# Kernel tuning notes

Measured on AMD Instinct MI355X. Metric: run time of the kernel, lower is better.

The kernel has to match this reference:

```python
import jax, jax.numpy as jnp
import numpy as np
import math

B = 16384
INPUT = 2048
HIDDEN = 2048
PROJ = 1024


def setup_inputs() -> dict:
    key = jax.random.key(0)
    ks = jax.random.split(key, 20)
    stdv = 1.0 / math.sqrt(PROJ)
    u = lambda k, shape: jax.random.uniform(k, shape, jnp.float32, -stdv, stdv)
    return {
        "x_t": jax.random.normal(ks[0], (B, INPUT), jnp.float32),
        "h_t": jax.random.normal(ks[1], (B, PROJ), jnp.float32),
        "c_t": jax.random.normal(ks[2], (B, HIDDEN), jnp.float32),
        "weight_if_x": u(ks[3], (INPUT, 2 * HIDDEN)),
        "weight_if_h": u(ks[4], (PROJ, 2 * HIDDEN)),
        "weight_if_c": u(ks[5], (HIDDEN, 2 * HIDDEN)),
        "bias_i": u(ks[6], (HIDDEN,)),
        "bias_f": u(ks[7], (HIDDEN,)),
        "weight_c_x": u(ks[8], (INPUT, HIDDEN)),
        "weight_c_h": u(ks[9], (PROJ, HIDDEN)),
        "bias_c": u(ks[10], (HIDDEN,)),
        "weight_o_x": u(ks[11], (INPUT, PROJ)),
        "weight_o_h": u(ks[12], (PROJ, PROJ)),
        "weight_o_c": u(ks[13], (HIDDEN, PROJ)),
        "bias_o": u(ks[14], (PROJ,)),
        "weight_r_proj": u(ks[15], (HIDDEN, PROJ)),
        "weight_r_x": u(ks[16], (INPUT, PROJ)),
    }


def reference(x_t, h_t, c_t, weight_if_x, weight_if_h, weight_if_c, bias_i, bias_f,
              weight_c_x, weight_c_h, bias_c, weight_o_x, weight_o_h, weight_o_c,
              bias_o, weight_r_proj, weight_r_x):
    # input/forget gates with peephole on c_t: [B, 2*HIDDEN]
    if_gates = x_t @ weight_if_x + h_t @ weight_if_h + c_t @ weight_if_c
    ingate, forgetgate = jnp.split(if_gates, 2, axis=-1)
    ingate = jax.nn.sigmoid(ingate + bias_i)
    forgetgate = jax.nn.sigmoid(forgetgate + bias_f)
    cellgate = jnp.tanh(x_t @ weight_c_x + h_t @ weight_c_h + bias_c)
    c_new = forgetgate * c_t + ingate * cellgate
    # output gate peeps at new cell state
    outgate = jax.nn.sigmoid(x_t @ weight_o_x + h_t @ weight_o_h + c_new @ weight_o_c + bias_o)
    r_t = jnp.tanh(c_new)
    m_t = r_t @ weight_r_proj
    # input_size != proj_size -> project x for the residual connection
    h_new = outgate * (m_t + x_t @ weight_r_x)
    return (h_new, c_new)
```

## Files before the change

kernel.cpp:

```cpp
#include <hip/hip_runtime.h>
#include <hip/hip_bf16.h>
#include <math.h>

typedef unsigned short u16;
typedef __bf16 bf16x8_t __attribute__((ext_vector_type(8)));
typedef float  f32x4_t  __attribute__((ext_vector_type(4)));
typedef float  f32x8_t  __attribute__((ext_vector_type(8)));
typedef float  f32x16_t __attribute__((ext_vector_type(16)));
typedef u16    u16x4_t  __attribute__((ext_vector_type(4)));
typedef u16    u16x8_t  __attribute__((ext_vector_type(8)));

__device__ __forceinline__ u16 f2b(float f) {
  unsigned u = __builtin_bit_cast(unsigned, f);
  u += 0x7fffu + ((u >> 16) & 1u);
  return (u16)(u >> 16);
}
__device__ __forceinline__ float b2f(u16 h) {
  unsigned u = ((unsigned)h) << 16;
  return __builtin_bit_cast(float, u);
}
__device__ __forceinline__ float sigm_(float x) { return 1.0f / (1.0f + __expf(-x)); }
__device__ __forceinline__ float tanh_(float x) { return 1.0f - 2.0f / (__expf(2.0f * x) + 1.0f); }

__device__ __forceinline__ void gload16(const void* g, void* l) {
  __builtin_amdgcn_global_load_lds(
      (__attribute__((address_space(1))) void*)(g),
      (__attribute__((address_space(3))) void*)(l), 16, 0, 0);
}


__global__ void cvt_act_kernel(const float* __restrict__ src, u16* __restrict__ dst,
                               int C, int KT, int c0) {
  int mb = blockIdx.x, ktl = blockIdx.y, t = threadIdx.x;
  int ktg = (c0 >> 5) + ktl;
  const float* s = src + (long)(mb * 256 + t) * C + ktl * 32;
  u16* d = dst + ((long)(mb * KT + ktg)) * 8192 + t * 8;
#pragma unroll
  for (int p = 0; p < 4; ++p) {
    f32x8_t v = *(const f32x8_t*)(s + p * 8);
    u16x8_t o;
#pragma unroll
    for (int r = 0; r < 8; ++r) o[r] = f2b(v[r]);
    *(u16x8_t*)(d + p * 2048) = o;
  }
}

__global__ void cvt_wt_kernel(const float* __restrict__ src, u16* __restrict__ dst,
                              int N, int KT, int n0, int k0) {
  int bx = blockIdx.x, by = blockIdx.y, t = threadIdx.x;
  int n = bx * 256 + t;
  int nb_g = (n0 >> 8) + bx;
  int ktg = (k0 >> 5) + by;
  float tmp[32];
#pragma unroll
  for (int kk = 0; kk < 32; ++kk)
    tmp[kk] = src[(long)(by * 32 + kk) * N + n];
  u16* d = dst + ((long)(nb_g * KT + ktg)) * 8192 + t * 8;
#pragma unroll
  for (int p = 0; p < 4; ++p) {
    u16x8_t o;
#pragma unroll
    for (int r = 0; r < 8; ++r) o[r] = f2b(tmp[p * 8 + r]);
    *(u16x8_t*)(d + p * 2048) = o;
  }
}

template <int MODE>
__global__ __launch_bounds__(512, 2) void gemm256_kernel(
    const u16* __restrict__ A, const u16* __restrict__ Bt, u16* __restrict__ Cout) {
  constexpr int KTF  = (MODE == 0) ? 160 : 128;
  constexpr int NCOL = (MODE == 0) ? 8192 : 2048;
  constexpr int NBN  = NCOL / 256;

  __shared__ u16 lds[2 * 32768];

  int bid = blockIdx.x;
  int cpx = gridDim.x >> 3;
  bid = (bid & 7) * cpx + (bid >> 3);

  int mb = bid / NBN, nb = bid % NBN;
  int m0 = mb * 256, n0 = nb * 256;

  int kt0, NT;
  if (MODE == 0) { kt0 = 0; NT = (nb < 16) ? 80 : ((nb < 28) ? 48 : 32); }
  else           { kt0 = (nb < 4) ? 0 : 64; NT = 32; }

  const int tid  = threadIdx.x;
  const int lane = tid & 63;
  const int wid  = tid >> 6;
  const int wr   = wid >> 2;
  const int wc   = wid & 3;
  const int l31  = lane & 31;
  const int hl   = lane >> 5;

  const int dstg = tid * 8;
  const u16* pA = A  + ((long)(mb * KTF + kt0)) * 8192 + dstg;
  const u16* pB = Bt + ((long)(nb * KTF + kt0)) * 8192 + dstg;

#define STG(bufb, tt, g) do { \
    gload16(pA + ((long)(2 * (tt))) * 8192 + (g) * 4096, \
            &lds[(bufb) * 32768 + (g) * 4096 + dstg]); \
    gload16(pB + ((long)(2 * (tt))) * 8192 + (g) * 4096, \
            &lds[(bufb) * 32768 + 16384 + (g) * 4096 + dstg]); } while (0)

  const int xbase = (wr * 128 + l31) * 8;
  const int wbase = (wc * 64  + l31) * 8;

  struct Frag { bf16x8_t x0, x1, x2, x3, w0, w1; };
  Frag fA, fB;

#define RD(F, sbp, ks) do { \
    const u16* _t = (sbp) + (2 * (ks) + hl) * 2048; \
    F.x0 = *(const bf16x8_t*)(_t + xbase); \
    F.x1 = *(const bf16x8_t*)(_t + xbase + 256); \
    F.x2 = *(const bf16x8_t*)(_t + xbase + 512); \
    F.x3 = *(const bf16x8_t*)(_t + xbase + 768); \
    F.w0 = *(const bf16x8_t*)(_t + 16384 + wbase); \
    F.w1 = *(const bf16x8_t*)(_t + 16384 + wbase + 256); } while (0)

#define MM(F) do { \
    acc[0][0] = __builtin_amdgcn_mfma_f32_32x32x16_bf16(F.w0, F.x0, acc[0][0], 0, 0, 0); \
    acc[0][1] = __builtin_amdgcn_mfma_f32_32x32x16_bf16(F.w1, F.x0, acc[0][1], 0, 0, 0); \
    acc[1][0] = __builtin_amdgcn_mfma_f32_32x32x16_bf16(F.w0, F.x1, acc[1][0], 0, 0, 0); \
    acc[1][1] = __builtin_amdgcn_mfma_f32_32x32x16_bf16(F.w1, F.x1, acc[1][1], 0, 0, 0); \
    acc[2][0] = __builtin_amdgcn_mfma_f32_32x32x16_bf16(F.w0, F.x2, acc[2][0], 0, 0, 0); \
    acc[2][1] = __builtin_amdgcn_mfma_f32_32x32x16_bf16(F.w1, F.x2, acc[2][1], 0, 0, 0); \
    acc[3][0] = __builtin_amdgcn_mfma_f32_32x32x16_bf16(F.w0, F.x3, acc[3][0], 0, 0, 0); \
    acc[3][1] = __builtin_amdgcn_mfma_f32_32x32x16_bf16(F.w1, F.x3, acc[3][1], 0, 0, 0); } while (0)

  f32x16_t acc[4][2];
#pragma unroll
  for (int m = 0; m < 4; ++m)
#pragma unroll
    for (int n = 0; n < 2; ++n)
#pragma unroll
      for (int r = 0; r < 16; ++r) acc[m][n][r] = 0.f;

  STG(0, 0, 0); STG(0, 0, 1); STG(0, 0, 2); STG(0, 0, 3);
  asm volatile("s_waitcnt vmcnt(0)" ::: "memory");
  __builtin_amdgcn_s_barrier();

  for (int t = 0; t < NT; ++t) {
    const int buf = t & 1;
    const u16* sb = &lds[buf * 32768];
    const bool pre = (t + 1 < NT);

    RD(fA, sb, 0);
    RD(fB, sb, 1);
    if (pre) { STG(buf ^ 1, t + 1, 0); STG(buf ^ 1, t + 1, 1); }
    __builtin_amdgcn_s_setprio(1); MM(fA); __builtin_amdgcn_s_setprio(0);
    RD(fA, sb, 2);
    if (pre) { STG(buf ^ 1, t + 1, 2); STG(buf ^ 1, t + 1, 3); }
    __builtin_amdgcn_s_setprio(1); MM(fB); __builtin_amdgcn_s_setprio(0);
    RD(fB, sb, 3);
    __builtin_amdgcn_s_setprio(1); MM(fA); __builtin_amdgcn_s_setprio(0);
    __builtin_amdgcn_s_setprio(1); MM(fB); __builtin_amdgcn_s_setprio(0);

    asm volatile("s_waitcnt vmcnt(0)" ::: "memory");
    __builtin_amdgcn_s_barrier();
  }
#undef STG
#undef RD
#undef MM

  const long rowg = (long)(m0 + wr * 128 + l31);
  const int  colg = n0 + wc * 64 + 4 * hl;
#pragma unroll
  for (int mm = 0; mm < 4; ++mm) {
    long rb = (rowg + mm * 32) * (long)NCOL;
#pragma unroll
    for (int nn = 0; nn < 2; ++nn) {
#pragma unroll
      for (int g = 0; g < 4; ++g) {
        u16x4_t o;
#pragma unroll
        for (int r = 0; r < 4; ++r) o[r] = f2b(acc[mm][nn][g * 4 + r]);
        *(u16x4_t*)&Cout[rb + colg + nn * 32 + g * 8] = o;
      }
    }
  }
}

__global__ void pass2_kernel(const u16* __restrict__ G1, const float* __restrict__ c_t,
                             const float* __restrict__ bias_i, const float* __restrict__ bias_f,
                             const float* __restrict__ bias_c,
                             float* __restrict__ c_new_out, u16* __restrict__ A2p) {
  int mb = blockIdx.x, jg = blockIdx.y, t = threadIdx.x;
  int b = mb * 256 + t;
  int j0 = jg * 32;
  const u16* row = G1 + (long)b * 8192 + j0;
  const float* cp_p = c_t + (long)b * 2048 + j0;
  float* co_p = c_new_out + (long)b * 2048 + j0;
  u16* dc = A2p + ((long)(mb * 128 + jg)) * 8192 + t * 8;
  u16* dr = dc + (long)64 * 8192;

#pragma unroll
  for (int q = 0; q < 4; ++q) {
    u16x8_t ip = *(const u16x8_t*)(row + q * 8);
    u16x8_t fp = *(const u16x8_t*)(row + 2048 + q * 8);
    u16x8_t gp = *(const u16x8_t*)(row + 4096 + q * 8);
    f32x8_t cp = *(const f32x8_t*)(cp_p + q * 8);
    f32x8_t bi = *(const f32x8_t*)(bias_i + j0 + q * 8);
    f32x8_t bf = *(const f32x8_t*)(bias_f + j0 + q * 8);
    f32x8_t bc = *(const f32x8_t*)(bias_c + j0 + q * 8);
    f32x8_t cn;
    u16x8_t cb, rb;
#pragma unroll
    for (int r = 0; r < 8; ++r) {
      float ig = sigm_(b2f(ip[r]) + bi[r]);
      float fg = sigm_(b2f(fp[r]) + bf[r]);
      float g  = tanh_(b2f(gp[r]) + bc[r]);
      float c  = fg * cp[r] + ig * g;
      cn[r] = c;
      cb[r] = f2b(c);
      rb[r] = f2b(tanh_(c));
    }
    *(f32x8_t*)(co_p + q * 8) = cn;
    *(u16x8_t*)(dc + q * 2048) = cb;
    *(u16x8_t*)(dr + q * 2048) = rb;
  }
}

__global__ void pass3_kernel(const u16* __restrict__ G1, const u16* __restrict__ G2,
                             const float* __restrict__ bias_o, float* __restrict__ h_out) {
  long i = (long)blockIdx.x * blockDim.x + threadIdx.x;
  long e = i * 8;
  int b = (int)(e >> 10);
  int j = (int)(e & 1023);
  const u16* row1 = G1 + (long)b * 8192;
  const u16* row2 = G2 + (long)b * 2048;
  u16x8_t ogp = *(const u16x8_t*)(row1 + 6144 + j);
  u16x8_t xrp = *(const u16x8_t*)(row1 + 7168 + j);
  u16x8_t ocg = *(const u16x8_t*)(row2 + j);
  u16x8_t mt  = *(const u16x8_t*)(row2 + 1024 + j);
  f32x8_t bo  = *(const f32x8_t*)(bias_o + j);
  f32x8_t h;
#pragma unroll
  for (int r = 0; r < 8; ++r) {
    float og = sigm_(b2f(ogp[r]) + b2f(ocg[r]) + bo[r]);
    h[r] = og * (b2f(mt[r]) + b2f(xrp[r]));
  }
  *(f32x8_t*)(h_out + (long)b * 1024 + j) = h;
}

extern "C" void kernel_launch(void* const* d_in, const int* in_sizes, int n_in,
                              void* d_out, int out_size, void* d_ws, size_t ws_size,
                              hipStream_t stream) {
  const float* x_t      = (const float*)d_in[0];
  const float* h_t      = (const float*)d_in[1];
  const float* c_t      = (const float*)d_in[2];
  const float* w_if_x   = (const float*)d_in[3];
  const float* w_if_h   = (const float*)d_in[4];
  const float* w_if_c   = (const float*)d_in[5];
  const float* bias_i   = (const float*)d_in[6];
  const float* bias_f   = (const float*)d_in[7];
  const float* w_c_x    = (const float*)d_in[8];
  const float* w_c_h    = (const float*)d_in[9];
  const float* bias_c   = (const float*)d_in[10];
  const float* w_o_x    = (const float*)d_in[11];
  const float* w_o_h    = (const float*)d_in[12];
  const float* w_o_c    = (const float*)d_in[13];
  const float* bias_o   = (const float*)d_in[14];
  const float* w_r_proj = (const float*)d_in[15];
  const float* w_r_x    = (const float*)d_in[16];

  char* ws = (char*)d_ws;
  u16* A1p  = (u16*)(ws);
  u16* W1tp = (u16*)(ws + 167772160L);
  u16* G1   = (u16*)(ws + 251658240L);
  u16* W2tp = (u16*)(ws + 520093696L);
  u16* A2p  = (u16*)(ws);
  u16* G2   = (u16*)(ws + 167772160L);

  float* h_out = (float*)d_out;
  float* c_out = h_out + 16384L * 1024L;

  cvt_act_kernel<<<dim3(64, 64), 256, 0, stream>>>(x_t, A1p, 2048, 160, 0);
  cvt_act_kernel<<<dim3(64, 32), 256, 0, stream>>>(h_t, A1p, 1024, 160, 2048);
  cvt_act_kernel<<<dim3(64, 64), 256, 0, stream>>>(c_t, A1p, 2048, 160, 3072);

  cvt_wt_kernel<<<dim3(16, 64), 256, 0, stream>>>(w_if_x,   W1tp, 4096, 160, 0,    0);
  cvt_wt_kernel<<<dim3(16, 32), 256, 0, stream>>>(w_if_h,   W1tp, 4096, 160, 0,    2048);
  cvt_wt_kernel<<<dim3(16, 64), 256, 0, stream>>>(w_if_c,   W1tp, 4096, 160, 0,    3072);
  cvt_wt_kernel<<<dim3(8,  64), 256, 0, stream>>>(w_c_x,    W1tp, 2048, 160, 4096, 0);
  cvt_wt_kernel<<<dim3(8,  32), 256, 0, stream>>>(w_c_h,    W1tp, 2048, 160, 4096, 2048);
  cvt_wt_kernel<<<dim3(4,  64), 256, 0, stream>>>(w_o_x,    W1tp, 1024, 160, 6144, 0);
  cvt_wt_kernel<<<dim3(4,  32), 256, 0, stream>>>(w_o_h,    W1tp, 1024, 160, 6144, 2048);
  cvt_wt_kernel<<<dim3(4,  64), 256, 0, stream>>>(w_r_x,    W1tp, 1024, 160, 7168, 0);
  cvt_wt_kernel<<<dim3(4,  64), 256, 0, stream>>>(w_o_c,    W2tp, 1024, 128, 0,    0);
  cvt_wt_kernel<<<dim3(4,  64), 256, 0, stream>>>(w_r_proj, W2tp, 1024, 128, 1024, 2048);

  gemm256_kernel<0><<<2048, 512, 0, stream>>>(A1p, W1tp, G1);

  pass2_kernel<<<dim3(64, 64), 256, 0, stream>>>(G1, c_t, bias_i, bias_f, bias_c, c_out, A2p);

  gemm256_kernel<1><<<512, 512, 0, stream>>>(A2p, W2tp, G2);

  pass3_kernel<<<8192, 256, 0, stream>>>(G1, G2, bias_o, h_out);
}
```

Measured before the change: 1.634 ms.

## Stream B fragments from global into registers; triple-buffer A tiles in LDS

Each wave now loads its B-operand fragments straight from global memory into registers, one k-step ahead, instead of staging them through LDS. Only the A operand goes through LDS, in a three-slot ring prefetched two steps ahead with partial vmcnt waits. Each iteration now covers a single k-tile instead of two. This cuts LDS footprint and LDS read traffic for B, but waves sharing a column block fetch the same B data redundantly from global, and there are twice as many barriers.

New measurement: 1.723 ms. 1.05x slower.

```diff
diff --git a/kernel.cpp b/kernel.cpp
--- a/kernel.cpp
+++ b/kernel.cpp
@@ -72,7 +72,7 @@
   constexpr int NCOL = (MODE == 0) ? 8192 : 2048;
   constexpr int NBN  = NCOL / 256;
 
-  __shared__ u16 lds[2 * 32768];
+  __shared__ u16 lds[3 * 8192];
 
   int bid = blockIdx.x;
   int cpx = gridDim.x >> 3;
@@ -82,8 +82,8 @@
   int m0 = mb * 256, n0 = nb * 256;
 
   int kt0, NT;
-  if (MODE == 0) { kt0 = 0; NT = (nb < 16) ? 80 : ((nb < 28) ? 48 : 32); }
-  else           { kt0 = (nb < 4) ? 0 : 64; NT = 32; }
+  if (MODE == 0) { kt0 = 0; NT = (nb < 16) ? 160 : ((nb < 28) ? 96 : 64); }
+  else           { kt0 = (nb < 4) ? 0 : 64; NT = 64; }
 
   const int tid  = threadIdx.x;
   const int lane = tid & 63;
@@ -94,39 +94,10 @@
   const int hl   = lane >> 5;
 
   const int dstg = tid * 8;
-  const u16* pA = A  + ((long)(mb * KTF + kt0)) * 8192 + dstg;
-  const u16* pB = Bt + ((long)(nb * KTF + kt0)) * 8192 + dstg;
-
-#define STG(bufb, tt, g) do { \
-    gload16(pA + ((long)(2 * (tt))) * 8192 + (g) * 4096, \
-            &lds[(bufb) * 32768 + (g) * 4096 + dstg]); \
-    gload16(pB + ((long)(2 * (tt))) * 8192 + (g) * 4096, \
-            &lds[(bufb) * 32768 + 16384 + (g) * 4096 + dstg]); } while (0)
-
-  const int xbase = (wr * 128 + l31) * 8;
-  const int wbase = (wc * 64  + l31) * 8;
-
-  struct Frag { bf16x8_t x0, x1, x2, x3, w0, w1; };
-  Frag fA, fB;
-
-#define RD(F, sbp, ks) do { \
-    const u16* _t = (sbp) + (2 * (ks) + hl) * 2048; \
-    F.x0 = *(const bf16x8_t*)(_t + xbase); \
-    F.x1 = *(const bf16x8_t*)(_t + xbase + 256); \
-    F.x2 = *(const bf16x8_t*)(_t + xbase + 512); \
-    F.x3 = *(const bf16x8_t*)(_t + xbase + 768); \
-    F.w0 = *(const bf16x8_t*)(_t + 16384 + wbase); \
-    F.w1 = *(const bf16x8_t*)(_t + 16384 + wbase + 256); } while (0)
-
-#define MM(F) do { \
-    acc[0][0] = __builtin_amdgcn_mfma_f32_32x32x16_bf16(F.w0, F.x0, acc[0][0], 0, 0, 0); \
-    acc[0][1] = __builtin_amdgcn_mfma_f32_32x32x16_bf16(F.w1, F.x0, acc[0][1], 0, 0, 0); \
-    acc[1][0] = __builtin_amdgcn_mfma_f32_32x32x16_bf16(F.w0, F.x1, acc[1][0], 0, 0, 0); \
-    acc[1][1] = __builtin_amdgcn_mfma_f32_32x32x16_bf16(F.w1, F.x1, acc[1][1], 0, 0, 0); \
-    acc[2][0] = __builtin_amdgcn_mfma_f32_32x32x16_bf16(F.w0, F.x2, acc[2][0], 0, 0, 0); \
-    acc[2][1] = __builtin_amdgcn_mfma_f32_32x32x16_bf16(F.w1, F.x2, acc[2][1], 0, 0, 0); \
-    acc[3][0] = __builtin_amdgcn_mfma_f32_32x32x16_bf16(F.w0, F.x3, acc[3][0], 0, 0, 0); \
-    acc[3][1] = __builtin_amdgcn_mfma_f32_32x32x16_bf16(F.w1, F.x3, acc[3][1], 0, 0, 0); } while (0)
+  const u16* pA = A + ((long)(mb * KTF + kt0)) * 8192 + dstg;
+
+  const u16* pBr = Bt + ((long)(nb * KTF + kt0)) * 8192
+                 + hl * 2048 + (wc * 64 + l31) * 8;
 
   f32x16_t acc[4][2];
 #pragma unroll
@@ -136,32 +107,76 @@
 #pragma unroll
       for (int r = 0; r < 16; ++r) acc[m][n][r] = 0.f;
 
-  STG(0, 0, 0); STG(0, 0, 1); STG(0, 0, 2); STG(0, 0, 3);
+  bf16x8_t bA[4], bB[4];
+
+  gload16(pA,        &lds[dstg]);
+  gload16(pA + 4096, &lds[4096 + dstg]);
+  gload16(pA + 8192,        &lds[8192 + dstg]);
+  gload16(pA + 8192 + 4096, &lds[8192 + 4096 + dstg]);
+  bA[0] = *(const bf16x8_t*)(pBr);
+  bA[1] = *(const bf16x8_t*)(pBr + 256);
+  bA[2] = *(const bf16x8_t*)(pBr + 4096);
+  bA[3] = *(const bf16x8_t*)(pBr + 4096 + 256);
   asm volatile("s_waitcnt vmcnt(0)" ::: "memory");
   __builtin_amdgcn_s_barrier();
 
-  for (int t = 0; t < NT; ++t) {
-    const int buf = t & 1;
-    const u16* sb = &lds[buf * 32768];
-    const bool pre = (t + 1 < NT);
-
-    RD(fA, sb, 0);
-    RD(fB, sb, 1);
-    if (pre) { STG(buf ^ 1, t + 1, 0); STG(buf ^ 1, t + 1, 1); }
-    __builtin_amdgcn_s_setprio(1); MM(fA); __builtin_amdgcn_s_setprio(0);
-    RD(fA, sb, 2);
-    if (pre) { STG(buf ^ 1, t + 1, 2); STG(buf ^ 1, t + 1, 3); }
-    __builtin_amdgcn_s_setprio(1); MM(fB); __builtin_amdgcn_s_setprio(0);
-    RD(fB, sb, 3);
-    __builtin_amdgcn_s_setprio(1); MM(fA); __builtin_amdgcn_s_setprio(0);
-    __builtin_amdgcn_s_setprio(1); MM(fB); __builtin_amdgcn_s_setprio(0);
-
-    asm volatile("s_waitcnt vmcnt(0)" ::: "memory");
-    __builtin_amdgcn_s_barrier();
-  }
-#undef STG
-#undef RD
-#undef MM
+  int _slot = 0, _s2 = 2;
+
+#define ITER(TT, CUR, NXT) do { \
+    const int _t = (TT); \
+    const u16* _sb = &lds[_slot * 8192]; \
+    const bool _p1 = (_t + 1 < NT), _p2 = (_t + 2 < NT); \
+    if (_p1) { \
+      const u16* _pb = pBr + (long)(_t + 1) * 8192; \
+      NXT[0] = *(const bf16x8_t*)(_pb); \
+      NXT[1] = *(const bf16x8_t*)(_pb + 256); \
+      NXT[2] = *(const bf16x8_t*)(_pb + 4096); \
+      NXT[3] = *(const bf16x8_t*)(_pb + 4096 + 256); \
+    } \
+    if (_p2) { \
+      gload16(pA + (long)(_t + 2) * 8192,        &lds[_s2 * 8192 + dstg]); \
+      gload16(pA + (long)(_t + 2) * 8192 + 4096, &lds[_s2 * 8192 + 4096 + dstg]); \
+    } \
+    bf16x8_t _a0, _a1, _a2, _a3; \
+    _a0 = *(const bf16x8_t*)(_sb + hl * 2048 + (wr * 128 + l31) * 8); \
+    _a1 = *(const bf16x8_t*)(_sb + hl * 2048 + (wr * 128 + 32 + l31) * 8); \
+    _a2 = *(const bf16x8_t*)(_sb + hl * 2048 + (wr * 128 + 64 + l31) * 8); \
+    _a3 = *(const bf16x8_t*)(_sb + hl * 2048 + (wr * 128 + 96 + l31) * 8); \
+    __builtin_amdgcn_s_setprio(1); \
+    acc[0][0] = __builtin_amdgcn_mfma_f32_32x32x16_bf16(CUR[0], _a0, acc[0][0], 0, 0, 0); \
+    acc[0][1] = __builtin_amdgcn_mfma_f32_32x32x16_bf16(CUR[1], _a0, acc[0][1], 0, 0, 0); \
+    acc[1][0] = __builtin_amdgcn_mfma_f32_32x32x16_bf16(CUR[0], _a1, acc[1][0], 0, 0, 0); \
+    acc[1][1] = __builtin_amdgcn_mfma_f32_32x32x16_bf16(CUR[1], _a1, acc[1][1], 0, 0, 0); \
+    acc[2][0] = __builtin_amdgcn_mfma_f32_32x32x16_bf16(CUR[0], _a2, acc[2][0], 0, 0, 0); \
+    acc[2][1] = __builtin_amdgcn_mfma_f32_32x32x16_bf16(CUR[1], _a2, acc[2][1], 0, 0, 0); \
+    acc[3][0] = __builtin_amdgcn_mfma_f32_32x32x16_bf16(CUR[0], _a3, acc[3][0], 0, 0, 0); \
+    acc[3][1] = __builtin_amdgcn_mfma_f32_32x32x16_bf16(CUR[1], _a3, acc[3][1], 0, 0, 0); \
+    _a0 = *(const bf16x8_t*)(_sb + (2 + hl) * 2048 + (wr * 128 + l31) * 8); \
+    _a1 = *(const bf16x8_t*)(_sb + (2 + hl) * 2048 + (wr * 128 + 32 + l31) * 8); \
+    _a2 = *(const bf16x8_t*)(_sb + (2 + hl) * 2048 + (wr * 128 + 64 + l31) * 8); \
+    _a3 = *(const bf16x8_t*)(_sb + (2 + hl) * 2048 + (wr * 128 + 96 + l31) * 8); \
+    acc[0][0] = __builtin_amdgcn_mfma_f32_32x32x16_bf16(CUR[2], _a0, acc[0][0], 0, 0, 0); \
+    acc[0][1] = __builtin_amdgcn_mfma_f32_32x32x16_bf16(CUR[3], _a0, acc[0][1], 0, 0, 0); \
+    acc[1][0] = __builtin_amdgcn_mfma_f32_32x32x16_bf16(CUR[2], _a1, acc[1][0], 0, 0, 0); \
+    acc[1][1] = __builtin_amdgcn_mfma_f32_32x32x16_bf16(CUR[3], _a1, acc[1][1], 0, 0, 0); \
+    acc[2][0] = __builtin_amdgcn_mfma_f32_32x32x16_bf16(CUR[2], _a2, acc[2][0], 0, 0, 0); \
+    acc[2][1] = __builtin_amdgcn_mfma_f32_32x32x16_bf16(CUR[3], _a2, acc[2][1], 0, 0, 0); \
+    acc[3][0] = __builtin_amdgcn_mfma_f32_32x32x16_bf16(CUR[2], _a3, acc[3][0], 0, 0, 0); \
+    acc[3][1] = __builtin_amdgcn_mfma_f32_32x32x16_bf16(CUR[3], _a3, acc[3][1], 0, 0, 0); \
+    __builtin_amdgcn_s_setprio(0); \
+    if (_p2)      asm volatile("s_waitcnt vmcnt(6)" ::: "memory"); \
+    else if (_p1) asm volatile("s_waitcnt vmcnt(4)" ::: "memory"); \
+    else          asm volatile("s_waitcnt vmcnt(0)" ::: "memory"); \
+    __builtin_amdgcn_s_barrier(); \
+    _slot = (_slot == 2) ? 0 : _slot + 1; \
+    _s2   = (_s2   == 2) ? 0 : _s2   + 1; \
+  } while (0)
+
+  for (int t = 0; t < NT; t += 2) {
+    ITER(t,     bA, bB);
+    ITER(t + 1, bB, bA);
+  }
+#undef ITER
 
   const long rowg = (long)(m0 + wr * 128 + l31);
   const int  colg = n0 + wc * 64 + 4 * hl;
```
